# Optimization experiments

Hardware: AMD Instinct MI355X
Metric: run time of the kernel (lower is better)

The kernel has to match this reference:

```python
import jax, jax.numpy as jnp
import numpy as np

N_NODES = 100000
N_EDGES = 3200000
D_IN, D_HID, D_OUT = 128, 64, 64


def setup_inputs() -> dict:
    key = jax.random.key(0)
    ks = jax.random.split(key, 8)
    x = jax.random.normal(ks[0], (N_NODES, D_IN), dtype=jnp.float32)
    edge_index = jax.random.randint(ks[1], (2, N_EDGES), 0, N_NODES, dtype=jnp.int32)
    # Glorot-ish init for GCN weights, zero bias (PyG default)
    def w(k, fi, fo):
        s = (6.0 / (fi + fo)) ** 0.5
        return jax.random.uniform(k, (fi, fo), jnp.float32, -s, s)
    return {
        "x": x,
        "edge_index": edge_index,
        "W1": w(ks[2], D_IN, D_HID), "b1": jnp.zeros((D_HID,), jnp.float32),
        "W2": w(ks[3], D_HID, D_HID), "b2": jnp.zeros((D_HID,), jnp.float32),
        "W3": w(ks[4], D_HID, D_OUT), "b3": jnp.zeros((D_OUT,), jnp.float32),
    }


def _gcn_layer(x, W, b, src, dst, norm, num_nodes):
    # GCNConv: out[i] = sum_{j->i} norm_ji * (x W)[j] + b   (self-loops included in src/dst)
    h = x @ W                                   # [N, F_out] small GEMM
    msg = h[src] * norm[:, None]                # [E+N, F_out] gather
    out = jax.ops.segment_sum(msg, dst, num_segments=num_nodes)  # scatter-add
    return out + b


def reference(x, edge_index, W1, b1, W2, b2, W3, b3):
    n = x.shape[0]
    loop = jnp.arange(n, dtype=edge_index.dtype)
    src = jnp.concatenate([edge_index[0], loop])  # add self-loops (GCN default)
    dst = jnp.concatenate([edge_index[1], loop])
    # symmetric normalization: deg^{-1/2}[src] * deg^{-1/2}[dst]
    deg = jax.ops.segment_sum(jnp.ones_like(dst, dtype=x.dtype), dst, num_segments=n)
    dinv = jnp.where(deg > 0, jax.lax.rsqrt(deg), 0.0)
    norm = dinv[src] * dinv[dst]

    h = jax.nn.relu(_gcn_layer(x, W1, b1, src, dst, norm, n))
    h = jax.nn.relu(_gcn_layer(h, W2, b2, src, dst, norm, n))
    out = _gcn_layer(h, W3, b3, src, dst, norm, n)
    return out
```

## Files before the change

kernel.cpp:

```cpp
#include <hip/hip_runtime.h>
#include <hip/hip_bf16.h>

static inline size_t align256(size_t x) { return (x + 255) & ~(size_t)255; }

#define BSTRIDE 9216


__global__ void cursor_init_kernel(int* __restrict__ cursor, int nb) {
    int b = blockIdx.x * blockDim.x + threadIdx.x;
    if (b < nb) cursor[b] = b * BSTRIDE;
}

__global__ __launch_bounds__(1024) void partition_place_kernel(const int* __restrict__ src,
                                                               const int* __restrict__ dst,
                                                               int* __restrict__ cursor,
                                                               unsigned int* __restrict__ part,
                                                               int e, int nb, int tile) {
    __shared__ int hist[512];
    __shared__ int base[512];
    const int t = threadIdx.x;
    const int lo = blockIdx.x * tile;
    const int hi = min(lo + tile, e);
    for (int i = t; i < nb; i += 1024) hist[i] = 0;
    __syncthreads();
    for (int i = lo + t; i < hi; i += 1024) atomicAdd(&hist[dst[i] >> 8], 1);
    __syncthreads();
    for (int i = t; i < nb; i += 1024) {
        int c = hist[i];
        base[i] = c ? atomicAdd(&cursor[i], c) : 0;
        hist[i] = 0;
    }
    __syncthreads();
    for (int i = lo + t; i < hi; i += 1024) {
        int s = src[i], d = dst[i];
        int b = d >> 8;
        int p = base[b] + atomicAdd(&hist[b], 1);
        part[p] = ((unsigned int)s << 8) | (unsigned int)(d & 255);
    }
}

__global__ __launch_bounds__(512) void cursor_scan_kernel(const int* __restrict__ cursor,
                                                          int* __restrict__ bstart, int nb) {
    __shared__ int lds[512];
    const int t = threadIdx.x;
    int v = (t < nb) ? (cursor[t] - t * BSTRIDE) : 0;
    lds[t] = v;
    __syncthreads();
    for (int off = 1; off < 512; off <<= 1) {
        int add = (t >= off) ? lds[t - off] : 0;
        __syncthreads();
        lds[t] += add;
        __syncthreads();
    }
    if (t < nb) {
        bstart[t] = lds[t] - v;
        if (t == nb - 1) bstart[nb] = lds[t];
    }
}

__global__ __launch_bounds__(1024) void csr_build_place_kernel(const unsigned int* __restrict__ part,
                                                               const int* __restrict__ bstart,
                                                               int* __restrict__ row_ptr,
                                                               float* __restrict__ dinv,
                                                               int* __restrict__ col, int n) {
    __shared__ int cnt[256];
    __shared__ int scan[256];
    __shared__ int cur[256];
    const int t = threadIdx.x;
    const int node0 = blockIdx.x << 8;
    const int o0 = bstart[blockIdx.x];
    const int m = bstart[blockIdx.x + 1] - o0;
    const int p0 = blockIdx.x * BSTRIDE;
    if (t < 256) cnt[t] = 0;
    __syncthreads();
    for (int i = t; i < m; i += 1024) atomicAdd(&cnt[part[p0 + i] & 255u], 1);
    __syncthreads();
    const int v = (t < 256) ? cnt[t] : 0;
    if (t < 256) scan[t] = v;
    __syncthreads();
    for (int off = 1; off < 256; off <<= 1) {
        int add = (t >= off && t < 256) ? scan[t - off] : 0;
        __syncthreads();
        if (t < 256) scan[t] += add;
        __syncthreads();
    }
    if (t < 256) {
        const int node = node0 + t;
        const int excl = o0 + scan[t] - v;
        cur[t] = excl;
        if (node < n) {
            row_ptr[node] = excl;
            dinv[node] = rsqrtf((float)(v + 1));
            if (node == n - 1) row_ptr[n] = o0 + m;
        }
    }
    __syncthreads();
    for (int i = t; i < m; i += 1024) {
        unsigned int sd = part[p0 + i];
        int p = atomicAdd(&cur[sd & 255u], 1);
        col[p] = (int)(sd >> 8);
    }
}


__device__ __forceinline__ unsigned int bf16rne(float f) {
    unsigned int u = __float_as_uint(f);
    return (u + 0x7fffu + ((u >> 16) & 1u)) >> 16;
}
__device__ __forceinline__ unsigned int bf16pack(float a, float b) {
    return bf16rne(a) | (bf16rne(b) << 16);
}
__device__ __forceinline__ void bf4add(float4& a, uint2 v) {
    float2 lo = __bfloat1622float2(*(const __hip_bfloat162*)&v.x);
    float2 hi = __bfloat1622float2(*(const __hip_bfloat162*)&v.y);
    a.x += lo.x; a.y += lo.y; a.z += hi.x; a.w += hi.y;
}


template<int K>
__global__ __launch_bounds__(256) void gemm_scale(const float* __restrict__ A,
                                                  const float* __restrict__ W,
                                                  const float* __restrict__ dinv,
                                                  unsigned int* __restrict__ gout, int n) {
    constexpr int KC = 64;
    constexpr int ROWS = 128;
    constexpr int LDX = KC + 4;
    __shared__ float xs[ROWS * LDX];
    __shared__ float ws[KC * 64];
    const int t = threadIdx.x;
    const int r0 = blockIdx.x * ROWS;
    const int rt = t >> 3;
    const int c4 = (t & 7) * 2;

    float acc[4][8];
#pragma unroll
    for (int a = 0; a < 4; ++a)
#pragma unroll
        for (int b = 0; b < 8; ++b) acc[a][b] = 0.f;

    for (int kc = 0; kc < K; kc += KC) {
        {
            const float4* Wg = (const float4*)(W + kc * 64);
            for (int i = t; i < KC * 16; i += 256) ((float4*)ws)[i] = Wg[i];
        }
        {
            const int jr = t >> 4;
            const int j = t & 15;
            for (int r = jr; r < ROWS; r += 16) {
                const int gr = r0 + r;
                float4 v = make_float4(0.f, 0.f, 0.f, 0.f);
                if (gr < n) v = ((const float4*)A)[(size_t)gr * (K / 4) + (kc >> 2) + j];
                *(float4*)&xs[r * LDX + j * 4] = v;
            }
        }
        __syncthreads();
#pragma unroll 4
        for (int k = 0; k < KC; ++k) {
            const float4 w0 = ((const float4*)ws)[k * 16 + c4];
            const float4 w1 = ((const float4*)ws)[k * 16 + c4 + 1];
#pragma unroll
            for (int rr = 0; rr < 4; ++rr) {
                const float xv = xs[(rt + rr * 32) * LDX + k];
                acc[rr][0] = fmaf(xv, w0.x, acc[rr][0]);
                acc[rr][1] = fmaf(xv, w0.y, acc[rr][1]);
                acc[rr][2] = fmaf(xv, w0.z, acc[rr][2]);
                acc[rr][3] = fmaf(xv, w0.w, acc[rr][3]);
                acc[rr][4] = fmaf(xv, w1.x, acc[rr][4]);
                acc[rr][5] = fmaf(xv, w1.y, acc[rr][5]);
                acc[rr][6] = fmaf(xv, w1.z, acc[rr][6]);
                acc[rr][7] = fmaf(xv, w1.w, acc[rr][7]);
            }
        }
        __syncthreads();
    }
#pragma unroll
    for (int rr = 0; rr < 4; ++rr) {
        const int gr = r0 + rt + rr * 32;
        if (gr < n) {
            const float d = dinv[gr];
            uint4 o;
            o.x = bf16pack(acc[rr][0] * d, acc[rr][1] * d);
            o.y = bf16pack(acc[rr][2] * d, acc[rr][3] * d);
            o.z = bf16pack(acc[rr][4] * d, acc[rr][5] * d);
            o.w = bf16pack(acc[rr][6] * d, acc[rr][7] * d);
            ((uint4*)gout)[(size_t)gr * 8 + (t & 7)] = o;
        }
    }
}


__device__ __forceinline__ float4 gather_agg(const uint2* __restrict__ g,
                                             const int* __restrict__ row_ptr,
                                             const int* __restrict__ col,
                                             int node, int fc) {
    float4 acc = make_float4(0.f, 0.f, 0.f, 0.f);
    bf4add(acc, g[(size_t)node * 16 + fc]);
    const int e0 = row_ptr[node];
    const int e1 = row_ptr[node + 1];
    int e = e0;
    for (; e + 16 <= e1; e += 16) {
        int s[16];
#pragma unroll
        for (int j = 0; j < 16; ++j) s[j] = col[e + j];
        uint2 v[16];
#pragma unroll
        for (int j = 0; j < 16; ++j) v[j] = g[(size_t)s[j] * 16 + fc];
#pragma unroll
        for (int j = 0; j < 16; ++j) bf4add(acc, v[j]);
    }
    for (; e + 8 <= e1; e += 8) {
        int s[8];
#pragma unroll
        for (int j = 0; j < 8; ++j) s[j] = col[e + j];
        uint2 v[8];
#pragma unroll
        for (int j = 0; j < 8; ++j) v[j] = g[(size_t)s[j] * 16 + fc];
#pragma unroll
        for (int j = 0; j < 8; ++j) bf4add(acc, v[j]);
    }
    for (; e < e1; ++e) bf4add(acc, g[(size_t)col[e] * 16 + fc]);
    return acc;
}


__global__ __launch_bounds__(256) void fused_agg_gemm_kernel(const uint2* __restrict__ g,
                                                             const int* __restrict__ row_ptr,
                                                             const int* __restrict__ col,
                                                             const float* __restrict__ dinv,
                                                             const float* __restrict__ bias,
                                                             const float* __restrict__ W,
                                                             unsigned int* __restrict__ gout,
                                                             int n) {
    __shared__ float ws[64 * 64];
    __shared__ float hs[16 * 68];
    const int t = threadIdx.x;
    const int r = t >> 4;
    const int fc = t & 15;
    const int node = blockIdx.x * 16 + r;
    const bool valid = node < n;

    for (int i = t; i < 1024; i += 256) ((float4*)ws)[i] = ((const float4*)W)[i];

    float4 acc = make_float4(0.f, 0.f, 0.f, 0.f);
    if (valid) {
        acc = gather_agg(g, row_ptr, col, node, fc);
        const float d = dinv[node];
        const float4 b = ((const float4*)bias)[fc];
        acc.x = fmaxf(fmaf(acc.x, d, b.x), 0.f);
        acc.y = fmaxf(fmaf(acc.y, d, b.y), 0.f);
        acc.z = fmaxf(fmaf(acc.z, d, b.z), 0.f);
        acc.w = fmaxf(fmaf(acc.w, d, b.w), 0.f);
    }
    *(float4*)&hs[r * 68 + fc * 4] = acc;
    __syncthreads();

    float a0 = 0.f, a1 = 0.f, a2 = 0.f, a3 = 0.f;
#pragma unroll 8
    for (int k = 0; k < 64; ++k) {
        const float hv = hs[r * 68 + k];
        const float4 wv = ((const float4*)ws)[k * 16 + fc];
        a0 = fmaf(hv, wv.x, a0);
        a1 = fmaf(hv, wv.y, a1);
        a2 = fmaf(hv, wv.z, a2);
        a3 = fmaf(hv, wv.w, a3);
    }
    if (valid) {
        const float d2 = dinv[node];
        uint2 o;
        o.x = bf16pack(a0 * d2, a1 * d2);
        o.y = bf16pack(a2 * d2, a3 * d2);
        ((uint2*)gout)[(size_t)node * 16 + fc] = o;
    }
}


__global__ __launch_bounds__(256) void aggregate_kernel(const uint2* __restrict__ g,
                                                        const int* __restrict__ row_ptr,
                                                        const int* __restrict__ col,
                                                        const float* __restrict__ dinv,
                                                        const float* __restrict__ bias,
                                                        float4* __restrict__ out,
                                                        int n) {
    const int t = threadIdx.x;
    const int node = blockIdx.x * 16 + (t >> 4);
    const int fc = t & 15;
    if (node >= n) return;
    float4 acc = gather_agg(g, row_ptr, col, node, fc);
    const float d = dinv[node];
    const float4 b = ((const float4*)bias)[fc];
    float4 o;
    o.x = fmaf(acc.x, d, b.x);
    o.y = fmaf(acc.y, d, b.y);
    o.z = fmaf(acc.z, d, b.z);
    o.w = fmaf(acc.w, d, b.w);
    out[(size_t)node * 16 + fc] = o;
}


extern "C" void kernel_launch(void* const* d_in, const int* in_sizes, int n_in,
                              void* d_out, int out_size, void* d_ws, size_t ws_size,
                              hipStream_t stream) {
    const float* x  = (const float*)d_in[0];
    const int*   ei = (const int*)d_in[1];
    const float* W1 = (const float*)d_in[2];
    const float* b1 = (const float*)d_in[3];
    const float* W2 = (const float*)d_in[4];
    const float* b2 = (const float*)d_in[5];
    const float* W3 = (const float*)d_in[6];
    const float* b3 = (const float*)d_in[7];
    float* out = (float*)d_out;

    const int n = in_sizes[0] / 128;
    const int e = in_sizes[1] / 2;
    const int* srcv = ei;
    const int* dstv = ei + e;

    char* ws = (char*)d_ws;
    size_t off = 0;
    float* dinv   = (float*)(ws + off); off = align256(off + (size_t)n * 4);
    int* row_ptr  = (int*)(ws + off);   off = align256(off + (size_t)(n + 1) * 4);
    int* bstart   = (int*)(ws + off);   off = align256(off + 1024 * 4);
    int* cursor   = (int*)(ws + off);   off = align256(off + 1024 * 4);
    int* col      = (int*)(ws + off);   off = align256(off + (size_t)e * 4);
    unsigned int* gbuf  = (unsigned int*)(ws + off); off = align256(off + (size_t)n * 64 * 2);
    unsigned int* gbuf2 = (unsigned int*)(ws + off); off = align256(off + (size_t)n * 64 * 2);
    unsigned int* part  = gbuf;
    (void)ws_size; (void)n_in; (void)out_size;

    const int nbkt = (n + 255) >> 8;

    cursor_init_kernel<<<2, 512, 0, stream>>>(cursor, nbkt);
    const int G = 400;
    const int tile = (e + G - 1) / G;
    partition_place_kernel<<<G, 1024, 0, stream>>>(srcv, dstv, cursor, part, e, nbkt, tile);
    cursor_scan_kernel<<<1, 512, 0, stream>>>(cursor, bstart, nbkt);
    csr_build_place_kernel<<<nbkt, 1024, 0, stream>>>(part, bstart, row_ptr, dinv, col, n);

    const int gemm_grid = (n + 127) / 128;
    const int agg_grid = (n + 15) / 16;

    gemm_scale<128><<<gemm_grid, 256, 0, stream>>>(x, W1, dinv, gbuf, n);
    fused_agg_gemm_kernel<<<agg_grid, 256, 0, stream>>>((const uint2*)gbuf, row_ptr, col,
                                                        dinv, b1, W2, gbuf2, n);
    fused_agg_gemm_kernel<<<agg_grid, 256, 0, stream>>>((const uint2*)gbuf2, row_ptr, col,
                                                        dinv, b2, W3, gbuf, n);
    aggregate_kernel<<<agg_grid, 256, 0, stream>>>((const uint2*)gbuf, row_ptr, col,
                                                   dinv, b3, (float4*)out, n);
}
```

Baseline: 410.1 us.

## Gather 8 bf16 features per lane with 16-byte loads and vectorized column reads

Aggregation now assigns 8 lanes per node, each loading a 16-byte uint4 of bf16 features instead of 16 lanes loading 8 bytes, so each block covers 32 nodes. Column indices are read as int4 after an alignment prologue, and accumulation uses packed float2 vectors, which may allow packed adds. This halves the lanes per node and doubles the nodes per wave, aiming for fewer gather instructions and more memory-level parallelism. In exchange each lane carries more registers and the unroll depth drops from 16 to 8 edges per iteration.

```diff
diff --git a/kernel.cpp b/kernel.cpp
--- a/kernel.cpp
+++ b/kernel.cpp
@@ -4,6 +4,8 @@
 static inline size_t align256(size_t x) { return (x + 255) & ~(size_t)255; }
 
 #define BSTRIDE 9216
+
+typedef float vf2 __attribute__((ext_vector_type(2)));
 
 
 __global__ void cursor_init_kernel(int* __restrict__ cursor, int nb) {
@@ -110,10 +112,17 @@
 __device__ __forceinline__ unsigned int bf16pack(float a, float b) {
     return bf16rne(a) | (bf16rne(b) << 16);
 }
-__device__ __forceinline__ void bf4add(float4& a, uint2 v) {
-    float2 lo = __bfloat1622float2(*(const __hip_bfloat162*)&v.x);
-    float2 hi = __bfloat1622float2(*(const __hip_bfloat162*)&v.y);
-    a.x += lo.x; a.y += lo.y; a.z += hi.x; a.w += hi.y;
+
+__device__ __forceinline__ vf2 bf2f(unsigned int u) {
+    float2 f = __bfloat1622float2(*(const __hip_bfloat162*)&u);
+    vf2 r; r.x = f.x; r.y = f.y;
+    return r;
+}
+__device__ __forceinline__ void bf8add(vf2* a, uint4 v) {
+    a[0] += bf2f(v.x);
+    a[1] += bf2f(v.y);
+    a[2] += bf2f(v.z);
+    a[3] += bf2f(v.w);
 }
 
 
@@ -189,41 +198,42 @@
 }
 
 
-__device__ __forceinline__ float4 gather_agg(const uint2* __restrict__ g,
-                                             const int* __restrict__ row_ptr,
-                                             const int* __restrict__ col,
-                                             int node, int fc) {
-    float4 acc = make_float4(0.f, 0.f, 0.f, 0.f);
-    bf4add(acc, g[(size_t)node * 16 + fc]);
-    const int e0 = row_ptr[node];
+__device__ __forceinline__ void gather_agg8(const uint4* __restrict__ g,
+                                            const int* __restrict__ row_ptr,
+                                            const int* __restrict__ col,
+                                            int node, int fc, vf2* acc) {
+    bf8add(acc, g[(size_t)node * 8 + fc]);
+    int e = row_ptr[node];
     const int e1 = row_ptr[node + 1];
-    int e = e0;
-    for (; e + 16 <= e1; e += 16) {
-        int s[16];
-#pragma unroll
-        for (int j = 0; j < 16; ++j) s[j] = col[e + j];
-        uint2 v[16];
-#pragma unroll
-        for (int j = 0; j < 16; ++j) v[j] = g[(size_t)s[j] * 16 + fc];
-#pragma unroll
-        for (int j = 0; j < 16; ++j) bf4add(acc, v[j]);
-    }
+    while (e < e1 && (e & 3)) { bf8add(acc, g[(size_t)col[e] * 8 + fc]); ++e; }
     for (; e + 8 <= e1; e += 8) {
-        int s[8];
-#pragma unroll
-        for (int j = 0; j < 8; ++j) s[j] = col[e + j];
-        uint2 v[8];
-#pragma unroll
-        for (int j = 0; j < 8; ++j) v[j] = g[(size_t)s[j] * 16 + fc];
-#pragma unroll
-        for (int j = 0; j < 8; ++j) bf4add(acc, v[j]);
-    }
-    for (; e < e1; ++e) bf4add(acc, g[(size_t)col[e] * 16 + fc]);
-    return acc;
-}
-
-
-__global__ __launch_bounds__(256) void fused_agg_gemm_kernel(const uint2* __restrict__ g,
+        const int4 c0 = *(const int4*)(col + e);
+        const int4 c1 = *(const int4*)(col + e + 4);
+        uint4 v0 = g[(size_t)c0.x * 8 + fc];
+        uint4 v1 = g[(size_t)c0.y * 8 + fc];
+        uint4 v2 = g[(size_t)c0.z * 8 + fc];
+        uint4 v3 = g[(size_t)c0.w * 8 + fc];
+        uint4 v4 = g[(size_t)c1.x * 8 + fc];
+        uint4 v5 = g[(size_t)c1.y * 8 + fc];
+        uint4 v6 = g[(size_t)c1.z * 8 + fc];
+        uint4 v7 = g[(size_t)c1.w * 8 + fc];
+        bf8add(acc, v0); bf8add(acc, v1); bf8add(acc, v2); bf8add(acc, v3);
+        bf8add(acc, v4); bf8add(acc, v5); bf8add(acc, v6); bf8add(acc, v7);
+    }
+    if (e + 4 <= e1) {
+        const int4 c0 = *(const int4*)(col + e);
+        uint4 v0 = g[(size_t)c0.x * 8 + fc];
+        uint4 v1 = g[(size_t)c0.y * 8 + fc];
+        uint4 v2 = g[(size_t)c0.z * 8 + fc];
+        uint4 v3 = g[(size_t)c0.w * 8 + fc];
+        bf8add(acc, v0); bf8add(acc, v1); bf8add(acc, v2); bf8add(acc, v3);
+        e += 4;
+    }
+    for (; e < e1; ++e) bf8add(acc, g[(size_t)col[e] * 8 + fc]);
+}
+
+
+__global__ __launch_bounds__(256) void fused_agg_gemm_kernel(const uint4* __restrict__ g,
                                                              const int* __restrict__ row_ptr,
                                                              const int* __restrict__ col,
                                                              const float* __restrict__ dinv,
@@ -232,49 +242,65 @@
                                                              unsigned int* __restrict__ gout,
                                                              int n) {
     __shared__ float ws[64 * 64];
-    __shared__ float hs[16 * 68];
-    const int t = threadIdx.x;
-    const int r = t >> 4;
-    const int fc = t & 15;
-    const int node = blockIdx.x * 16 + r;
+    __shared__ float hs[32 * 68];
+    const int t = threadIdx.x;
+    const int r = t >> 3;
+    const int fc = t & 7;
+    const int node = blockIdx.x * 32 + r;
     const bool valid = node < n;
 
     for (int i = t; i < 1024; i += 256) ((float4*)ws)[i] = ((const float4*)W)[i];
 
-    float4 acc = make_float4(0.f, 0.f, 0.f, 0.f);
+    vf2 acc[4];
+    acc[0] = vf2{0.f, 0.f}; acc[1] = vf2{0.f, 0.f};
+    acc[2] = vf2{0.f, 0.f}; acc[3] = vf2{0.f, 0.f};
     if (valid) {
-        acc = gather_agg(g, row_ptr, col, node, fc);
+        gather_agg8(g, row_ptr, col, node, fc, acc);
         const float d = dinv[node];
-        const float4 b = ((const float4*)bias)[fc];
-        acc.x = fmaxf(fmaf(acc.x, d, b.x), 0.f);
-        acc.y = fmaxf(fmaf(acc.y, d, b.y), 0.f);
-        acc.z = fmaxf(fmaf(acc.z, d, b.z), 0.f);
-        acc.w = fmaxf(fmaf(acc.w, d, b.w), 0.f);
-    }
-    *(float4*)&hs[r * 68 + fc * 4] = acc;
+        const float4 b0 = ((const float4*)bias)[fc * 2];
+        const float4 b1 = ((const float4*)bias)[fc * 2 + 1];
+        acc[0].x = fmaxf(fmaf(acc[0].x, d, b0.x), 0.f);
+        acc[0].y = fmaxf(fmaf(acc[0].y, d, b0.y), 0.f);
+        acc[1].x = fmaxf(fmaf(acc[1].x, d, b0.z), 0.f);
+        acc[1].y = fmaxf(fmaf(acc[1].y, d, b0.w), 0.f);
+        acc[2].x = fmaxf(fmaf(acc[2].x, d, b1.x), 0.f);
+        acc[2].y = fmaxf(fmaf(acc[2].y, d, b1.y), 0.f);
+        acc[3].x = fmaxf(fmaf(acc[3].x, d, b1.z), 0.f);
+        acc[3].y = fmaxf(fmaf(acc[3].y, d, b1.w), 0.f);
+    }
+    *(float4*)&hs[r * 68 + fc * 8]     = make_float4(acc[0].x, acc[0].y, acc[1].x, acc[1].y);
+    *(float4*)&hs[r * 68 + fc * 8 + 4] = make_float4(acc[2].x, acc[2].y, acc[3].x, acc[3].y);
     __syncthreads();
 
     float a0 = 0.f, a1 = 0.f, a2 = 0.f, a3 = 0.f;
+    float a4 = 0.f, a5 = 0.f, a6 = 0.f, a7 = 0.f;
 #pragma unroll 8
     for (int k = 0; k < 64; ++k) {
         const float hv = hs[r * 68 + k];
-        const float4 wv = ((const float4*)ws)[k * 16 + fc];
-        a0 = fmaf(hv, wv.x, a0);
-        a1 = fmaf(hv, wv.y, a1);
-        a2 = fmaf(hv, wv.z, a2);
-        a3 = fmaf(hv, wv.w, a3);
+        const float4 w0 = ((const float4*)ws)[k * 16 + fc * 2];
+        const float4 w1 = ((const float4*)ws)[k * 16 + fc * 2 + 1];
+        a0 = fmaf(hv, w0.x, a0);
+        a1 = fmaf(hv, w0.y, a1);
+        a2 = fmaf(hv, w0.z, a2);
+        a3 = fmaf(hv, w0.w, a3);
+        a4 = fmaf(hv, w1.x, a4);
+        a5 = fmaf(hv, w1.y, a5);
+        a6 = fmaf(hv, w1.z, a6);
+        a7 = fmaf(hv, w1.w, a7);
     }
     if (valid) {
         const float d2 = dinv[node];
-        uint2 o;
+        uint4 o;
         o.x = bf16pack(a0 * d2, a1 * d2);
         o.y = bf16pack(a2 * d2, a3 * d2);
-        ((uint2*)gout)[(size_t)node * 16 + fc] = o;
-    }
-}
-
-
-__global__ __launch_bounds__(256) void aggregate_kernel(const uint2* __restrict__ g,
+        o.z = bf16pack(a4 * d2, a5 * d2);
+        o.w = bf16pack(a6 * d2, a7 * d2);
+        ((uint4*)gout)[(size_t)node * 8 + fc] = o;
+    }
+}
+
+
+__global__ __launch_bounds__(256) void aggregate_kernel(const uint4* __restrict__ g,
                                                         const int* __restrict__ row_ptr,
                                                         const int* __restrict__ col,
                                                         const float* __restrict__ dinv,
@@ -282,18 +308,27 @@
                                                         float4* __restrict__ out,
                                                         int n) {
     const int t = threadIdx.x;
-    const int node = blockIdx.x * 16 + (t >> 4);
-    const int fc = t & 15;
+    const int node = blockIdx.x * 32 + (t >> 3);
+    const int fc = t & 7;
     if (node >= n) return;
-    float4 acc = gather_agg(g, row_ptr, col, node, fc);
+    vf2 acc[4];
+    acc[0] = vf2{0.f, 0.f}; acc[1] = vf2{0.f, 0.f};
+    acc[2] = vf2{0.f, 0.f}; acc[3] = vf2{0.f, 0.f};
+    gather_agg8(g, row_ptr, col, node, fc, acc);
     const float d = dinv[node];
-    const float4 b = ((const float4*)bias)[fc];
-    float4 o;
-    o.x = fmaf(acc.x, d, b.x);
-    o.y = fmaf(acc.y, d, b.y);
-    o.z = fmaf(acc.z, d, b.z);
-    o.w = fmaf(acc.w, d, b.w);
-    out[(size_t)node * 16 + fc] = o;
+    const float4 b0 = ((const float4*)bias)[fc * 2];
+    const float4 b1 = ((const float4*)bias)[fc * 2 + 1];
+    float4 o0, o1;
+    o0.x = fmaf(acc[0].x, d, b0.x);
+    o0.y = fmaf(acc[0].y, d, b0.y);
+    o0.z = fmaf(acc[1].x, d, b0.z);
+    o0.w = fmaf(acc[1].y, d, b0.w);
+    o1.x = fmaf(acc[2].x, d, b1.x);
+    o1.y = fmaf(acc[2].y, d, b1.y);
+    o1.z = fmaf(acc[3].x, d, b1.z);
+    o1.w = fmaf(acc[3].y, d, b1.w);
+    out[(size_t)node * 16 + fc * 2]     = o0;
+    out[(size_t)node * 16 + fc * 2 + 1] = o1;
 }
 
 
@@ -337,13 +372,13 @@
     csr_build_place_kernel<<<nbkt, 1024, 0, stream>>>(part, bstart, row_ptr, dinv, col, n);
 
     const int gemm_grid = (n + 127) / 128;
-    const int agg_grid = (n + 15) / 16;
+    const int agg_grid = (n + 31) / 32;
 
     gemm_scale<128><<<gemm_grid, 256, 0, stream>>>(x, W1, dinv, gbuf, n);
-    fused_agg_gemm_kernel<<<agg_grid, 256, 0, stream>>>((const uint2*)gbuf, row_ptr, col,
+    fused_agg_gemm_kernel<<<agg_grid, 256, 0, stream>>>((const uint4*)gbuf, row_ptr, col,
                                                         dinv, b1, W2, gbuf2, n);
-    fused_agg_gemm_kernel<<<agg_grid, 256, 0, stream>>>((const uint2*)gbuf2, row_ptr, col,
+    fused_agg_gemm_kernel<<<agg_grid, 256, 0, stream>>>((const uint4*)gbuf2, row_ptr, col,
                                                         dinv, b2, W3, gbuf, n);
-    aggregate_kernel<<<agg_grid, 256, 0, stream>>>((const uint2*)gbuf, row_ptr, col,
+    aggregate_kernel<<<agg_grid, 256, 0, stream>>>((const uint4*)gbuf, row_ptr, col,
                                                    dinv, b3, (float4*)out, n);
 }
```

Result: faster. 392.4 us, median of 2 (-4.3%).
